# Kernel tuning notes

Measured on AMD Instinct MI355X. Metric: run time of the kernel, lower is better.

The kernel has to match this reference:

```python
import jax, jax.numpy as jnp
import numpy as np

HID = 512      # hidden_size
IN = 1         # encoder/decoder input feature size
OUT = 1        # linear output size (feeds back as decoder input)
SEQ = 1000     # encoder sequence length
BATCH = 512
TGT = 1000     # target_len (decoder steps)


def setup_inputs() -> dict:
    key = jax.random.key(0)
    ks = jax.random.split(key, 11)
    s = 1.0 / np.sqrt(HID)  # PyTorch LSTM/Linear uniform init scale
    u = lambda k, shp: jax.random.uniform(k, shp, jnp.float32, -s, s)
    return {
        "input_batch": jax.random.normal(ks[0], (SEQ, BATCH, IN), jnp.float32),
        "enc_Wih": u(ks[1], (4 * HID, IN)),
        "enc_Whh": u(ks[2], (4 * HID, HID)),
        "enc_bih": u(ks[3], (4 * HID,)),
        "enc_bhh": u(ks[4], (4 * HID,)),
        "dec_Wih": u(ks[5], (4 * HID, OUT)),
        "dec_Whh": u(ks[6], (4 * HID, HID)),
        "dec_bih": u(ks[7], (4 * HID,)),
        "dec_bhh": u(ks[8], (4 * HID,)),
        "lin_W": u(ks[9], (OUT, HID)),
        "lin_b": u(ks[10], (OUT,)),
    }


def _lstm_cell(x, h, c, Wih, Whh, b):
    # PyTorch gate order: i, f, g, o
    gates = x @ Wih.T + h @ Whh.T + b  # [B, 4H]
    i, f, g, o = jnp.split(gates, 4, axis=-1)
    c = jax.nn.sigmoid(f) * c + jax.nn.sigmoid(i) * jnp.tanh(g)
    h = jax.nn.sigmoid(o) * jnp.tanh(c)
    return h, c


def reference(input_batch, enc_Wih, enc_Whh, enc_bih, enc_bhh,
              dec_Wih, dec_Whh, dec_bih, dec_bhh, lin_W, lin_b):
    batch = input_batch.shape[1]
    b_enc = enc_bih + enc_bhh
    b_dec = dec_bih + dec_bhh
    h0 = jnp.zeros((batch, HID), input_batch.dtype)

    # --- encoder: scan over SEQ time steps, zero initial state ---
    def enc_step(carry, x_t):
        h, c = carry
        h, c = _lstm_cell(x_t, h, c, enc_Wih, enc_Whh, b_enc)
        return (h, c), None

    (h, c), _ = jax.lax.scan(enc_step, (h0, h0), input_batch)

    x0 = jnp.zeros((batch, OUT), input_batch.dtype)

    def dec_step(carry, _):
        h, c, x = carry
        h, c = _lstm_cell(x, h, c, dec_Wih, dec_Whh, b_dec)
        pred = h @ lin_W.T + lin_b  # [B, OUT]
        return (h, c, pred), pred

    _, outputs = jax.lax.scan(dec_step, (h, c, x0), None, length=TGT)
    return outputs  # [TGT, BATCH, OUT]
```

## Files before the change

kernel.cpp:

```cpp
#include <hip/hip_runtime.h>


typedef _Float16 f16x8 __attribute__((ext_vector_type(8)));
typedef _Float16 f16x4 __attribute__((ext_vector_type(4)));
typedef float    f32x4 __attribute__((ext_vector_type(4)));
typedef unsigned long long u64;

#define GLOAD_LDS16(gp, lp)                                                    \
  __builtin_amdgcn_global_load_lds(                                            \
      (const __attribute__((address_space(1))) void*)(gp),                     \
      (__attribute__((address_space(3))) void*)(lp), 16, 0, 17)

__device__ __forceinline__ void store_h8_llc(_Float16* p, f16x4 v) {
  __hip_atomic_store((u64*)p, __builtin_bit_cast(u64, v),
                     __ATOMIC_RELAXED, __HIP_MEMORY_SCOPE_AGENT);
}

__device__ __forceinline__ float sigm(float x) {
  return __builtin_amdgcn_rcpf(1.0f + __expf(-x));
}
__device__ __forceinline__ float tanh_fast(float x) {
  float r = __expf(-2.0f*fabsf(x));
  float t = (1.0f - r)*__builtin_amdgcn_rcpf(1.0f + r);
  return copysignf(t, x);
}

__global__ void init_zero(float* __restrict__ out, int nout,
                          float* __restrict__ wsf, int nws) {
  int i = blockIdx.x*blockDim.x + threadIdx.x;
  int st = gridDim.x*blockDim.x;
  for (int j=i; j<nout; j+=st)
    __hip_atomic_store(&out[j], 0.f, __ATOMIC_RELAXED, __HIP_MEMORY_SCOPE_AGENT);
  for (int j=i; j<nws;  j+=st)
    __hip_atomic_store(&wsf[j], 0.f, __ATOMIC_RELAXED, __HIP_MEMORY_SCOPE_AGENT);
}

__global__ __launch_bounds__(256, 1) void lstm_main(
    const float* __restrict__ xin,
    const float* __restrict__ encWih, const float* __restrict__ encWhh,
    const float* __restrict__ enc_bih, const float* __restrict__ enc_bhh,
    const float* __restrict__ decWih, const float* __restrict__ decWhh,
    const float* __restrict__ dec_bih, const float* __restrict__ dec_bhh,
    const float* __restrict__ linW, const float* __restrict__ linb,
    float* __restrict__ out,
    _Float16* __restrict__ hbuf,
    int* __restrict__ flags)
{
  __shared__ f16x8 h_lds[4096];
  __shared__ float gates[64][68];

  const int bid = blockIdx.x, tid = threadIdx.x;
  const int rb = bid >> 5, hb = bid & 31;
  const int wid = tid >> 6, lane = tid & 63;
  const int wrow = wid >> 1, wcol = wid & 1;
  const int lcol = lane & 15, lq = lane >> 4, kq = lq*8;

  const int b_local = tid >> 2, u0 = (tid & 3)*4;
  const int bg = rb*64 + b_local;
  const int jh0 = hb*16 + u0;

  float linw[4];
  #pragma unroll
  for (int u=0; u<4; ++u) linw[u] = linW[jh0+u];
  const float linbv = linb[0];

  f16x8 wHi[2][16], wLo[2][16];
  float biasv[16], wihv[16];
  float c[4] = {0.f, 0.f, 0.f, 0.f};
  int* myflag = flags + (rb*32 + hb)*32;
  const int* pollp = flags + (rb*32 + (lane & 31))*32;

  int goff[16];
  #pragma unroll
  for (int i=0; i<16; ++i) {
    const int cch = i*256 + tid;
    const int pair = (cch >> 6) & 31;
    const int ks = pair >> 1, half = pair & 1;
    const int row_local = (cch >> 11)*32 + half*16 + lcol;
    goff[i] = row_local*512 + ks*32 + kq;
  }

  auto loadW = [&](const float* Whh, const float* bih, const float* bhh,
                   const float* Wih) {
    #pragma unroll
    for (int ct=0; ct<2; ++ct) {
      const int g = wcol*2 + ct;
      const float* wr = Whh + (size_t)(g*512 + hb*16 + lcol)*512;
      #pragma unroll
      for (int ks=0; ks<16; ++ks) {
        f16x8 hi, lo;
        #pragma unroll
        for (int i=0; i<8; ++i) {
          float w = wr[ks*32 + kq + i];
          _Float16 hh = (_Float16)w;
          float hf = (float)hh;
          float rem = (w - hf)*2048.0f;
          if (fabsf(hf) < 6.104e-5f) { hh = (_Float16)0.0f; rem = w*2048.0f; }
          hi[i] = hh; lo[i] = (_Float16)rem;
        }
        wHi[ct][ks] = hi; wLo[ct][ks] = lo;
      }
    }
    #pragma unroll
    for (int g=0; g<4; ++g) {
      #pragma unroll
      for (int u=0; u<4; ++u) {
        int j = g*512 + jh0 + u;
        biasv[g*4+u] = bih[j] + bhh[j];
        wihv[g*4+u]  = Wih[j];
      }
    }
  };

  loadW(encWhh, enc_bih, enc_bhh, encWih);

  for (int s=0; s<2000; ++s) {
    if (s == 1000) {
      loadW(decWhh, dec_bih, dec_bhh, decWih);
    }
    const bool dec = (s >= 1000);
    const int td = s - 1000;
    const _Float16* hr = hbuf + (size_t)((s+1)&1)*(512*512);
    _Float16*       hw = hbuf + (size_t)( s   &1)*(512*512);

    float x;
    if (!dec) x = xin[(size_t)s*512 + bg];
    else      x = (td > 0) ? __hip_atomic_load(&out[(size_t)(td-1)*512 + bg],
                                               __ATOMIC_RELAXED, __HIP_MEMORY_SCOPE_AGENT)
                           : 0.0f;

    const _Float16* hrb = hr + (size_t)rb*64*512;
    {
      f16x8* ldst = &h_lds[(size_t)wid*64];
      #pragma unroll
      for (int i=0; i<16; ++i)
        GLOAD_LDS16(hrb + goff[i], ldst + i*256);
    }
    __syncthreads();

    f32x4 accH[2][2], accL[2][2];
    #pragma unroll
    for (int rt=0; rt<2; ++rt)
      #pragma unroll
      for (int ctt=0; ctt<2; ++ctt) {
        accH[rt][ctt] = {0.f,0.f,0.f,0.f};
        accL[rt][ctt] = {0.f,0.f,0.f,0.f};
      }

    const f16x8* Ha = &h_lds[(size_t)wrow*2048];
    #pragma unroll
    for (int ks=0; ks<16; ++ks) {
      const f16x8 a0 = Ha[ks*128 + lane];
      const f16x8 a1 = Ha[ks*128 + 64 + lane];
      accH[0][0] = __builtin_amdgcn_mfma_f32_16x16x32_f16(a0, wHi[0][ks], accH[0][0], 0,0,0);
      accH[1][0] = __builtin_amdgcn_mfma_f32_16x16x32_f16(a1, wHi[0][ks], accH[1][0], 0,0,0);
      accH[0][1] = __builtin_amdgcn_mfma_f32_16x16x32_f16(a0, wHi[1][ks], accH[0][1], 0,0,0);
      accH[1][1] = __builtin_amdgcn_mfma_f32_16x16x32_f16(a1, wHi[1][ks], accH[1][1], 0,0,0);
      accL[0][0] = __builtin_amdgcn_mfma_f32_16x16x32_f16(a0, wLo[0][ks], accL[0][0], 0,0,0);
      accL[1][0] = __builtin_amdgcn_mfma_f32_16x16x32_f16(a1, wLo[0][ks], accL[1][0], 0,0,0);
      accL[0][1] = __builtin_amdgcn_mfma_f32_16x16x32_f16(a0, wLo[1][ks], accL[0][1], 0,0,0);
      accL[1][1] = __builtin_amdgcn_mfma_f32_16x16x32_f16(a1, wLo[1][ks], accL[1][1], 0,0,0);
    }

    #pragma unroll
    for (int rt=0; rt<2; ++rt) {
      #pragma unroll
      for (int ctt=0; ctt<2; ++ctt) {
        f32x4 v = accH[rt][ctt] + accL[rt][ctt]*(1.0f/2048.0f);
        const int col  = wcol*32 + ctt*16 + lcol;
        const int row0 = wrow*32 + rt*16 + lq*4;
        #pragma unroll
        for (int i=0; i<4; ++i) gates[row0+i][col] = v[i];
      }
    }
    __syncthreads();

    const f32x4 gi = *reinterpret_cast<const f32x4*>(&gates[b_local][ 0 + u0]);
    const f32x4 gf = *reinterpret_cast<const f32x4*>(&gates[b_local][16 + u0]);
    const f32x4 gg = *reinterpret_cast<const f32x4*>(&gates[b_local][32 + u0]);
    const f32x4 go = *reinterpret_cast<const f32x4*>(&gates[b_local][48 + u0]);

    f16x4 hv4;
    float sp = 0.f;
    #pragma unroll
    for (int u=0; u<4; ++u) {
      float ai = gi[u] + biasv[ 0+u] + x*wihv[ 0+u];
      float af = gf[u] + biasv[ 4+u] + x*wihv[ 4+u];
      float ag = gg[u] + biasv[ 8+u] + x*wihv[ 8+u];
      float ao = go[u] + biasv[12+u] + x*wihv[12+u];
      float iv = sigm(ai);
      float fv = sigm(af);
      float gv = tanh_fast(ag);
      float ov = sigm(ao);
      float cn = fv*c[u] + iv*gv;
      c[u] = cn;
      float hv = ov*tanh_fast(cn);
      hv4[u] = (_Float16)hv;
      sp += hv*linw[u];
    }
    store_h8_llc(hw + (size_t)bg*512 + jh0, hv4);

    if (dec) {
      sp += __shfl_xor(sp, 1);
      sp += __shfl_xor(sp, 2);
      if ((tid & 3) == 0) {
        float v = sp + (hb == 0 ? linbv : 0.f);
        __hip_atomic_fetch_add(&out[(size_t)td*512 + bg], v,
                               __ATOMIC_RELAXED, __HIP_MEMORY_SCOPE_AGENT);
      }
    }

    if (s != 1999) {
      asm volatile("s_waitcnt vmcnt(0)" ::: "memory");
      __syncthreads();
      const int target = s + 1;
      if (tid == 0)
        __hip_atomic_store(myflag, target, __ATOMIC_RELAXED, __HIP_MEMORY_SCOPE_AGENT);
      if (wid == 0) {
        while (!__all(__hip_atomic_load(pollp, __ATOMIC_RELAXED,
                                        __HIP_MEMORY_SCOPE_AGENT) >= target)) { }
      }
      __syncthreads();
    }
  }
}

extern "C" void kernel_launch(void* const* d_in, const int* in_sizes, int n_in,
                              void* d_out, int out_size, void* d_ws, size_t ws_size,
                              hipStream_t stream) {
  const float* xin     = (const float*)d_in[0];
  const float* encWih  = (const float*)d_in[1];
  const float* encWhh  = (const float*)d_in[2];
  const float* enc_bih = (const float*)d_in[3];
  const float* enc_bhh = (const float*)d_in[4];
  const float* decWih  = (const float*)d_in[5];
  const float* decWhh  = (const float*)d_in[6];
  const float* dec_bih = (const float*)d_in[7];
  const float* dec_bhh = (const float*)d_in[8];
  const float* linW    = (const float*)d_in[9];
  const float* linb    = (const float*)d_in[10];
  float* out = (float*)d_out;
  char* ws = (char*)d_ws;
  int* flags = (int*)ws;
  _Float16* hbuf = (_Float16*)(ws + 32768);

  init_zero<<<512, 256, 0, stream>>>(out, 1000*512, (float*)ws,
                                     (32768 + 2*512*512*2)/4);

  lstm_main<<<dim3(256), dim3(256), 0, stream>>>(
      xin, encWih, encWhh, enc_bih, enc_bhh,
      decWih, decWhh, dec_bih, dec_bhh,
      linW, linb, out, hbuf, flags);
}
```

Measured before the change: 13.73 ms.

## Split hidden-state LDS load in halves to overlap with MFMA; poll flags in all waves

The per-step load of the hidden state into LDS is split into two halves. MFMA work on the first half of K starts while the second half is still in flight, with a barrier between the two halves. The grid-barrier wait now has every wave poll the flag array, replacing wave 0 polling followed by a block barrier, which removes one __syncthreads per step. This trades more polling traffic to global memory and relies on the goff ordering matching the ks split.

```diff
diff --git a/kernel.cpp b/kernel.cpp
--- a/kernel.cpp
+++ b/kernel.cpp
@@ -102,41 +102,41 @@
       }
     }
     #pragma unroll
-    for (int g=0; g<4; ++g) {
+    for (int g=0; g<4; ++g)
       #pragma unroll
       for (int u=0; u<4; ++u) {
         int j = g*512 + jh0 + u;
         biasv[g*4+u] = bih[j] + bhh[j];
         wihv[g*4+u]  = Wih[j];
       }
-    }
   };
 
   loadW(encWhh, enc_bih, enc_bhh, encWih);
 
   for (int s=0; s<2000; ++s) {
-    if (s == 1000) {
-      loadW(decWhh, dec_bih, dec_bhh, decWih);
-    }
+    if (s == 1000) loadW(decWhh, dec_bih, dec_bhh, decWih);
     const bool dec = (s >= 1000);
     const int td = s - 1000;
     const _Float16* hr = hbuf + (size_t)((s+1)&1)*(512*512);
     _Float16*       hw = hbuf + (size_t)( s   &1)*(512*512);
 
+    const _Float16* hrb = hr + (size_t)rb*64*512;
+    f16x8* ldst = &h_lds[(size_t)wid*64];
+
     float x;
     if (!dec) x = xin[(size_t)s*512 + bg];
-    else      x = (td > 0) ? __hip_atomic_load(&out[(size_t)(td-1)*512 + bg],
-                                               __ATOMIC_RELAXED, __HIP_MEMORY_SCOPE_AGENT)
-                           : 0.0f;
-
-    const _Float16* hrb = hr + (size_t)rb*64*512;
-    {
-      f16x8* ldst = &h_lds[(size_t)wid*64];
-      #pragma unroll
-      for (int i=0; i<16; ++i)
-        GLOAD_LDS16(hrb + goff[i], ldst + i*256);
-    }
+    else if (td == 0) x = 0.0f;
+    else x = __hip_atomic_load(&out[(size_t)(td-1)*512 + bg],
+                               __ATOMIC_RELAXED, __HIP_MEMORY_SCOPE_AGENT);
+
+    #pragma unroll
+    for (int i=0; i<16; ++i)
+      if ((i & 7) < 4) GLOAD_LDS16(hrb + goff[i], ldst + i*256);
     __syncthreads();
+
+    #pragma unroll
+    for (int i=0; i<16; ++i)
+      if ((i & 7) >= 4) GLOAD_LDS16(hrb + goff[i], ldst + i*256);
 
     f32x4 accH[2][2], accL[2][2];
     #pragma unroll
@@ -146,10 +146,10 @@
         accH[rt][ctt] = {0.f,0.f,0.f,0.f};
         accL[rt][ctt] = {0.f,0.f,0.f,0.f};
       }
-
     const f16x8* Ha = &h_lds[(size_t)wrow*2048];
-    #pragma unroll
-    for (int ks=0; ks<16; ++ks) {
+
+    #pragma unroll
+    for (int ks=0; ks<8; ++ks) {
       const f16x8 a0 = Ha[ks*128 + lane];
       const f16x8 a1 = Ha[ks*128 + 64 + lane];
       accH[0][0] = __builtin_amdgcn_mfma_f32_16x16x32_f16(a0, wHi[0][ks], accH[0][0], 0,0,0);
@@ -161,9 +161,24 @@
       accL[0][1] = __builtin_amdgcn_mfma_f32_16x16x32_f16(a0, wLo[1][ks], accL[0][1], 0,0,0);
       accL[1][1] = __builtin_amdgcn_mfma_f32_16x16x32_f16(a1, wLo[1][ks], accL[1][1], 0,0,0);
     }
-
-    #pragma unroll
-    for (int rt=0; rt<2; ++rt) {
+    __syncthreads();
+
+    #pragma unroll
+    for (int ks=8; ks<16; ++ks) {
+      const f16x8 a0 = Ha[ks*128 + lane];
+      const f16x8 a1 = Ha[ks*128 + 64 + lane];
+      accH[0][0] = __builtin_amdgcn_mfma_f32_16x16x32_f16(a0, wHi[0][ks], accH[0][0], 0,0,0);
+      accH[1][0] = __builtin_amdgcn_mfma_f32_16x16x32_f16(a1, wHi[0][ks], accH[1][0], 0,0,0);
+      accH[0][1] = __builtin_amdgcn_mfma_f32_16x16x32_f16(a0, wHi[1][ks], accH[0][1], 0,0,0);
+      accH[1][1] = __builtin_amdgcn_mfma_f32_16x16x32_f16(a1, wHi[1][ks], accH[1][1], 0,0,0);
+      accL[0][0] = __builtin_amdgcn_mfma_f32_16x16x32_f16(a0, wLo[0][ks], accL[0][0], 0,0,0);
+      accL[1][0] = __builtin_amdgcn_mfma_f32_16x16x32_f16(a1, wLo[0][ks], accL[1][0], 0,0,0);
+      accL[0][1] = __builtin_amdgcn_mfma_f32_16x16x32_f16(a0, wLo[1][ks], accL[0][1], 0,0,0);
+      accL[1][1] = __builtin_amdgcn_mfma_f32_16x16x32_f16(a1, wLo[1][ks], accL[1][1], 0,0,0);
+    }
+
+    #pragma unroll
+    for (int rt=0; rt<2; ++rt)
       #pragma unroll
       for (int ctt=0; ctt<2; ++ctt) {
         f32x4 v = accH[rt][ctt] + accL[rt][ctt]*(1.0f/2048.0f);
@@ -172,7 +187,6 @@
         #pragma unroll
         for (int i=0; i<4; ++i) gates[row0+i][col] = v[i];
       }
-    }
     __syncthreads();
 
     const f32x4 gi = *reinterpret_cast<const f32x4*>(&gates[b_local][ 0 + u0]);
@@ -213,14 +227,11 @@
     if (s != 1999) {
       asm volatile("s_waitcnt vmcnt(0)" ::: "memory");
       __syncthreads();
-      const int target = s + 1;
+      const int av = s + 1;
       if (tid == 0)
-        __hip_atomic_store(myflag, target, __ATOMIC_RELAXED, __HIP_MEMORY_SCOPE_AGENT);
-      if (wid == 0) {
-        while (!__all(__hip_atomic_load(pollp, __ATOMIC_RELAXED,
-                                        __HIP_MEMORY_SCOPE_AGENT) >= target)) { }
-      }
-      __syncthreads();
+        __hip_atomic_store(myflag, av, __ATOMIC_RELAXED, __HIP_MEMORY_SCOPE_AGENT);
+      while (!__all(__hip_atomic_load(pollp, __ATOMIC_RELAXED,
+                                      __HIP_MEMORY_SCOPE_AGENT) >= av)) { }
     }
   }
 }
```

New measurement: 14.71 ms. 1.07x slower.
